# Performance work log

Measured on AMD Instinct MI355X. Metric: run time of the kernel, lower is better.

## Reference

```python
import jax, jax.numpy as jnp
import numpy as np

B, T, D, H, K = 8, 4096, 768, 12, 64
EPS_WKV = 1e-9
EPS_GN = 1e-5


def setup_inputs() -> dict:
    key = jax.random.key(0)
    ks = jax.random.split(key, 12)
    x = jax.random.normal(ks[0], (B, T, D), jnp.float32)
    # linear projection weights (torch nn.Linear stores [out, in]; y = x @ W.T)
    W_r = jax.random.normal(ks[1], (D, D), jnp.float32) * 0.02
    W_k = jax.random.normal(ks[2], (D, D), jnp.float32) * 0.02
    W_v = jax.random.normal(ks[3], (D, D), jnp.float32) * 0.02
    W_o = jax.random.normal(ks[4], (D, D), jnp.float32) * 0.02
    time_mix_r = jax.random.uniform(ks[5], (D,), jnp.float32)
    time_mix_k = jax.random.uniform(ks[6], (D,), jnp.float32)
    time_mix_v = jax.random.uniform(ks[7], (D,), jnp.float32)
    # around the module's init values (time_decay ~ -0.075, time_first ~ 0.15 at layer 6/12)
    time_decay = -0.075 + 0.1 * jax.random.normal(ks[8], (H, K), jnp.float32)
    time_first = 0.15 + 0.1 * jax.random.normal(ks[9], (H, K), jnp.float32)
    gn_weight = jnp.ones((D,), jnp.float32)
    gn_bias = jnp.zeros((D,), jnp.float32)
    return {
        "x": x,
        "time_mix_r": time_mix_r, "time_mix_k": time_mix_k, "time_mix_v": time_mix_v,
        "time_decay": time_decay, "time_first": time_first,
        "W_r": W_r, "W_k": W_k, "W_v": W_v, "W_o": W_o,
        "gn_weight": gn_weight, "gn_bias": gn_bias,
    }


def reference(x, time_mix_r, time_mix_k, time_mix_v, time_decay, time_first,
              W_r, W_k, W_v, W_o, gn_weight, gn_bias):
    Bx, Tx, Dx = x.shape
    Hx, Kx = time_decay.shape
    # token-shift: previous timestep (zero-initialized state)
    x_prev = jnp.concatenate([jnp.zeros_like(x[:, :1]), x[:, :-1]], axis=1)
    xr = x * time_mix_r + x_prev * (1.0 - time_mix_r)
    xk = x * time_mix_k + x_prev * (1.0 - time_mix_k)
    xv = x * time_mix_v + x_prev * (1.0 - time_mix_v)
    r = jax.nn.sigmoid(xr @ W_r.T).reshape(Bx, Tx, Hx, Kx)
    k = (xk @ W_k.T).reshape(Bx, Tx, Hx, Kx)
    v = (xv @ W_v.T).reshape(Bx, Tx, Hx, Kx)

    w = jnp.exp(-jnp.exp(time_decay))   # [H,K] decay per channel
    eu = jnp.exp(time_first)            # [H,K] bonus for current token

    def step(carry, kv_t):
        num, den = carry                # each [B,H,K]
        k_t, v_t = kv_t                 # each [B,H,K]
        ek = jnp.exp(k_t)
        wkv = (num + eu * ek * v_t) / (den + eu * ek + EPS_WKV)
        return (num * w + ek * v_t, den * w + ek), wkv

    k_tm = jnp.moveaxis(k, 1, 0)        # [T,B,H,K]
    v_tm = jnp.moveaxis(v, 1, 0)
    init = (jnp.zeros((Bx, Hx, Kx), x.dtype), jnp.zeros((Bx, Hx, Kx), x.dtype))
    _, wkv = jax.lax.scan(step, init, (k_tm, v_tm))
    out = jnp.moveaxis(wkv, 0, 1)       # [B,T,H,K]

    y = r * out                         # [B,T,H,K]
    # torch GroupNorm(H, D) on [B, D, T]: normalize each group over (K channels x T steps)
    mean = y.mean(axis=(1, 3), keepdims=True)
    var = y.var(axis=(1, 3), keepdims=True)
    y = (y - mean) * jax.lax.rsqrt(var + EPS_GN)
    y = y * gn_weight.reshape(1, 1, Hx, Kx) + gn_bias.reshape(1, 1, Hx, Kx)
    return y.reshape(Bx, Tx, Dx) @ W_o.T
```

## Files before the change

### kernel.cpp

```cpp
#include <hip/hip_runtime.h>
#include <hip/hip_bf16.h>
#include <cstdint>

#define B_ 8
#define T_ 4096
#define D_ 768
#define H_ 12
#define M_ (B_*T_)
#define CHUNKS 64
#define CLEN 64
#define WELEM (D_*D_)
#define NCH (B_*H_*64)

typedef __attribute__((ext_vector_type(8))) short bf16x8;
typedef __attribute__((ext_vector_type(4))) float f32x4;

static __device__ __forceinline__ unsigned short f2bf(float f) {
  __hip_bfloat16 h = __float2bfloat16(f);
  return __builtin_bit_cast(unsigned short, h);
}
static __device__ __forceinline__ float bf2f(unsigned short u) {
  unsigned v = ((unsigned)u) << 16;
  return __builtin_bit_cast(float, v);
}

static __device__ __forceinline__ void async16(const void* g, void* l) {
  __builtin_amdgcn_global_load_lds(
      (const __attribute__((address_space(1))) unsigned int*)g,
      (__attribute__((address_space(3))) unsigned int*)l, 16, 0, 0);
}

__global__ __launch_bounds__(256) void zero_out_kernel(float* __restrict__ out, size_t n4) {
  size_t gid = (size_t)blockIdx.x * 256 + threadIdx.x;
  if (gid < n4) *(float4*)(out + gid * 4) = make_float4(0.f, 0.f, 0.f, 0.f);
}

__global__ __launch_bounds__(256) void mix_kernel(
    const float* __restrict__ x, const float* __restrict__ tmr,
    const float* __restrict__ tmk, const float* __restrict__ tmv,
    unsigned short* __restrict__ xr, unsigned short* __restrict__ xk,
    unsigned short* __restrict__ xv) {
  size_t gid = (size_t)blockIdx.x * 256 + threadIdx.x;
  size_t idx4 = gid * 4;
  int d = (int)(idx4 % D_);
  size_t row = idx4 / D_;
  int t = (int)(row & (T_ - 1));
  float4 xc = *(const float4*)(x + idx4);
  float4 xp = make_float4(0.f, 0.f, 0.f, 0.f);
  if (t > 0) xp = *(const float4*)(x + idx4 - D_);
  float4 mr = *(const float4*)(tmr + d);
  float4 mk = *(const float4*)(tmk + d);
  float4 mv = *(const float4*)(tmv + d);
  ushort4 orr, okk, ovv;
  orr.x = f2bf(xc.x*mr.x + xp.x*(1.f-mr.x));
  orr.y = f2bf(xc.y*mr.y + xp.y*(1.f-mr.y));
  orr.z = f2bf(xc.z*mr.z + xp.z*(1.f-mr.z));
  orr.w = f2bf(xc.w*mr.w + xp.w*(1.f-mr.w));
  okk.x = f2bf(xc.x*mk.x + xp.x*(1.f-mk.x));
  okk.y = f2bf(xc.y*mk.y + xp.y*(1.f-mk.y));
  okk.z = f2bf(xc.z*mk.z + xp.z*(1.f-mk.z));
  okk.w = f2bf(xc.w*mk.w + xp.w*(1.f-mk.w));
  ovv.x = f2bf(xc.x*mv.x + xp.x*(1.f-mv.x));
  ovv.y = f2bf(xc.y*mv.y + xp.y*(1.f-mv.y));
  ovv.z = f2bf(xc.z*mv.z + xp.z*(1.f-mv.z));
  ovv.w = f2bf(xc.w*mv.w + xp.w*(1.f-mv.w));
  *(ushort4*)(xr + idx4) = orr;
  *(ushort4*)(xk + idx4) = okk;
  *(ushort4*)(xv + idx4) = ovv;
}

__global__ __launch_bounds__(256) void wconv_kernel(
    const float* __restrict__ a, const float* __restrict__ b,
    const float* __restrict__ c, const float* __restrict__ d,
    unsigned short* __restrict__ o) {
  size_t gid = (size_t)blockIdx.x * 256 + threadIdx.x;
  size_t idx4 = gid * 4;
  size_t mi = idx4 / WELEM;
  size_t off = idx4 % WELEM;
  const float* src = (mi == 0) ? a : (mi == 1) ? b : (mi == 2) ? c : d;
  float4 v = *(const float4*)(src + off);
  ushort4 u;
  u.x = f2bf(v.x); u.y = f2bf(v.y); u.z = f2bf(v.z); u.w = f2bf(v.w);
  *(ushort4*)(o + idx4) = u;
}

template<int ACT, int OBF>
__global__ __launch_bounds__(256) void gemm_nt(
    const unsigned short* __restrict__ A,
    const unsigned short* __restrict__ Bw,
    void* __restrict__ Cv, int M, int N, int Kd) {
  __shared__ __align__(16) unsigned short As[128 * 32];
  __shared__ __align__(16) unsigned short Bs[128 * 32];
  const int tid = threadIdx.x;
  const int wave = tid >> 6, lane = tid & 63;
  const int quad = lane >> 4, l16 = lane & 15;
  const int m0 = blockIdx.y * 128, n0 = blockIdx.x * 128;
  const int wm = (wave & 1) * 64, wn = (wave >> 1) * 64;

  f32x4 acc[4][4] = {};

  for (int kb = 0; kb < Kd; kb += 32) {
    __syncthreads();
#pragma unroll
    for (int j = 0; j < 2; ++j) {
      int chunk = wave * 128 + j * 64 + lane;
      int row = chunk >> 2, kc = chunk & 3;
      const unsigned short* ga = A  + ((size_t)(m0 + row) * Kd + kb + kc * 8);
      async16(ga, &As[chunk * 8]);
      const unsigned short* gb = Bw + ((size_t)(n0 + row) * Kd + kb + kc * 8);
      async16(gb, &Bs[chunk * 8]);
    }
    __syncthreads();

    bf16x8 a[4], b[4];
#pragma unroll
    for (int i = 0; i < 4; ++i)
      a[i] = *(const bf16x8*)&As[(wm + i * 16 + l16) * 32 + quad * 8];
#pragma unroll
    for (int i = 0; i < 4; ++i)
      b[i] = *(const bf16x8*)&Bs[(wn + i * 16 + l16) * 32 + quad * 8];
#pragma unroll
    for (int i = 0; i < 4; ++i)
#pragma unroll
      for (int j = 0; j < 4; ++j)
        acc[i][j] = __builtin_amdgcn_mfma_f32_16x16x32_bf16(a[i], b[j], acc[i][j], 0, 0, 0);
  }

#pragma unroll
  for (int i = 0; i < 4; ++i) {
    int rowb = m0 + wm + i * 16 + quad * 4;
#pragma unroll
    for (int j = 0; j < 4; ++j) {
      int col = n0 + wn + j * 16 + l16;
#pragma unroll
      for (int r = 0; r < 4; ++r) {
        float v = acc[i][j][r];
        if (ACT == 1) v = 1.f / (1.f + __expf(-v));
        size_t idx = (size_t)(rowb + r) * N + col;
        if (OBF) ((unsigned short*)Cv)[idx] = f2bf(v);
        else     ((float*)Cv)[idx] = v;
      }
    }
  }
}

__global__ __launch_bounds__(256) void wkv_pass1(
    const unsigned short* __restrict__ Kb, const unsigned short* __restrict__ Vb,
    const float* __restrict__ td,
    float* __restrict__ sumN, float* __restrict__ sumD) {
  int gid = blockIdx.x * 256 + threadIdx.x;
  int k = gid & 63;
  int h = (gid >> 6) % H_;
  int tmp = (gid >> 6) / H_;
  int b = tmp % B_;
  int c = tmp / B_;
  float w = __expf(-__expf(td[h * 64 + k]));
  size_t base = ((size_t)(b * T_ + c * CLEN)) * D_ + h * 64 + k;
  float num = 0.f, den = 0.f;
#pragma unroll 8
  for (int i = 0; i < CLEN; ++i) {
    float kk = bf2f(Kb[base + (size_t)i * D_]);
    float vv = bf2f(Vb[base + (size_t)i * D_]);
    float ek = __expf(kk);
    num = num * w + ek * vv;
    den = den * w + ek;
  }
  sumN[gid] = num;
  sumD[gid] = den;
}

__global__ __launch_bounds__(256) void wkv_pass2(
    const float* __restrict__ sumN, const float* __restrict__ sumD,
    const float* __restrict__ td,
    float* __restrict__ prefN, float* __restrict__ prefD,
    float* __restrict__ gstats) {
  int tid = blockIdx.x * 256 + threadIdx.x;
  if (blockIdx.x == 0 && threadIdx.x < 192) gstats[threadIdx.x] = 0.f;
  int k = tid & 63;
  int h = (tid >> 6) % H_;
  float w = __expf(-__expf(td[h * 64 + k]));
  float wL = w;
#pragma unroll
  for (int i = 0; i < 6; ++i) wL *= wL;
  float n = 0.f, d = 0.f;
  for (int c = 0; c < CHUNKS; ++c) {
    int j = c * NCH + tid;
    prefN[j] = n; prefD[j] = d;
    n = n * wL + sumN[j];
    d = d * wL + sumD[j];
  }
}

__global__ __launch_bounds__(256) void wkv_pass3(
    const unsigned short* __restrict__ Kb, const unsigned short* __restrict__ Vb,
    unsigned short* __restrict__ RY,
    const float* __restrict__ td, const float* __restrict__ tf,
    const float* __restrict__ prefN, const float* __restrict__ prefD,
    float* __restrict__ gsum, float* __restrict__ gsq) {
  int gid = blockIdx.x * 256 + threadIdx.x;
  int k = gid & 63;
  int h = (gid >> 6) % H_;
  int tmp = (gid >> 6) / H_;
  int b = tmp % B_;
  int c = tmp / B_;
  float w = __expf(-__expf(td[h * 64 + k]));
  float eu = __expf(tf[h * 64 + k]);
  float num = prefN[gid], den = prefD[gid];
  size_t base = ((size_t)(b * T_ + c * CLEN)) * D_ + h * 64 + k;
  float s1 = 0.f, s2 = 0.f;
#pragma unroll 4
  for (int i = 0; i < CLEN; ++i) {
    size_t idx = base + (size_t)i * D_;
    float kk = bf2f(Kb[idx]);
    float vv = bf2f(Vb[idx]);
    float rr = bf2f(RY[idx]);
    float ek = __expf(kk);
    float wkv = (num + eu * ek * vv) / (den + eu * ek + 1e-9f);
    unsigned short ybf = f2bf(rr * wkv);
    RY[idx] = ybf;
    float y = bf2f(ybf);
    s1 += y; s2 += y * y;
    num = num * w + ek * vv;
    den = den * w + ek;
  }
#pragma unroll
  for (int off = 32; off; off >>= 1) {
    s1 += __shfl_down(s1, off);
    s2 += __shfl_down(s2, off);
  }
  if (k == 0) {
    atomicAdd(&gsum[b * H_ + h], s1);
    atomicAdd(&gsq [b * H_ + h], s2);
  }
}

__global__ __launch_bounds__(256) void gn_kernel(
    const unsigned short* __restrict__ Y, const float* __restrict__ gsum,
    const float* __restrict__ gsq, const float* __restrict__ gw,
    const float* __restrict__ gb, unsigned short* __restrict__ Ybf) {
  size_t gid = (size_t)blockIdx.x * 256 + threadIdx.x;
  size_t idx4 = gid * 4;
  int d = (int)(idx4 % D_);
  size_t row = idx4 / D_;
  int b = (int)(row >> 12);
  int h = d >> 6;
  int g = b * H_ + h;
  const float inv = 1.f / (float)(T_ * 64);
  float mean = gsum[g] * inv;
  float var = gsq[g] * inv - mean * mean;
  float rstd = rsqrtf(var + 1e-5f);
  ushort4 yu = *(const ushort4*)(Y + idx4);
  float4 wv = *(const float4*)(gw + d);
  float4 bv = *(const float4*)(gb + d);
  ushort4 o;
  o.x = f2bf((bf2f(yu.x) - mean) * rstd * wv.x + bv.x);
  o.y = f2bf((bf2f(yu.y) - mean) * rstd * wv.y + bv.y);
  o.z = f2bf((bf2f(yu.z) - mean) * rstd * wv.z + bv.z);
  o.w = f2bf((bf2f(yu.w) - mean) * rstd * wv.w + bv.w);
  *(ushort4*)(Ybf + idx4) = o;
}

extern "C" void kernel_launch(void* const* d_in, const int* in_sizes, int n_in,
                              void* d_out, int out_size, void* d_ws, size_t ws_size,
                              hipStream_t stream) {
  (void)in_sizes; (void)n_in;
  const float* x   = (const float*)d_in[0];
  const float* tmr = (const float*)d_in[1];
  const float* tmk = (const float*)d_in[2];
  const float* tmv = (const float*)d_in[3];
  const float* td  = (const float*)d_in[4];
  const float* tf  = (const float*)d_in[5];
  const float* Wr  = (const float*)d_in[6];
  const float* Wk  = (const float*)d_in[7];
  const float* Wv  = (const float*)d_in[8];
  const float* Wo  = (const float*)d_in[9];
  const float* gw  = (const float*)d_in[10];
  const float* gb  = (const float*)d_in[11];
  float* out = (float*)d_out;

  constexpr size_t MD = (size_t)M_ * D_;
  constexpr size_t NEED = 4 * (MD * 2)
                        + (size_t)4 * WELEM * 2
                        + 4 * ((size_t)CHUNKS * NCH * 4)
                        + 1024;
  if (ws_size < NEED) {
    zero_out_kernel<<<(int)((MD / 4 + 255) / 256), 256, 0, stream>>>(out, MD / 4);
    return;
  }

  char* ws = (char*)d_ws;
  unsigned short* XR = (unsigned short*)ws; ws += MD * 2;
  unsigned short* XK = (unsigned short*)ws; ws += MD * 2;
  unsigned short* XV = (unsigned short*)ws; ws += MD * 2;
  unsigned short* Rb = (unsigned short*)ws; ws += MD * 2;
  unsigned short* Wb = (unsigned short*)ws; ws += (size_t)4 * WELEM * 2;
  float* sumN  = (float*)ws; ws += (size_t)CHUNKS * NCH * 4;
  float* sumD  = (float*)ws; ws += (size_t)CHUNKS * NCH * 4;
  float* prefN = (float*)ws; ws += (size_t)CHUNKS * NCH * 4;
  float* prefD = (float*)ws; ws += (size_t)CHUNKS * NCH * 4;
  float* gstats = (float*)ws; ws += 1024;
  unsigned short* Kb = XR;
  unsigned short* Vb = XK;
  unsigned short* Yb = XV;

  mix_kernel<<<(int)(MD / 1024), 256, 0, stream>>>(x, tmr, tmk, tmv, XR, XK, XV);
  wconv_kernel<<<(4 * WELEM / 4) / 256, 256, 0, stream>>>(Wr, Wk, Wv, Wo, Wb);

  dim3 ggrid(D_ / 128, M_ / 128);
  gemm_nt<1, 1><<<ggrid, 256, 0, stream>>>(XR, Wb,             Rb, M_, D_, D_);
  gemm_nt<0, 1><<<ggrid, 256, 0, stream>>>(XK, Wb + WELEM,     Kb, M_, D_, D_);
  gemm_nt<0, 1><<<ggrid, 256, 0, stream>>>(XV, Wb + 2 * WELEM, Vb, M_, D_, D_);

  wkv_pass1<<<(CHUNKS * NCH) / 256, 256, 0, stream>>>(Kb, Vb, td, sumN, sumD);
  wkv_pass2<<<NCH / 256, 256, 0, stream>>>(sumN, sumD, td, prefN, prefD, gstats);
  wkv_pass3<<<(CHUNKS * NCH) / 256, 256, 0, stream>>>(Kb, Vb, Rb, td, tf,
                                                      prefN, prefD, gstats, gstats + 96);
  gn_kernel<<<(int)(MD / 1024), 256, 0, stream>>>(Rb, gstats, gstats + 96, gw, gb, Yb);

  gemm_nt<0, 0><<<ggrid, 256, 0, stream>>>(Yb, Wb + 3 * WELEM, out, M_, D_, D_);
}
```

Before: 579.0 us.

## Double-buffer GEMM, interleave R/K/V into one buffer, split mix kernel

The GEMM now double-buffers its LDS tiles with async global-to-LDS loads and explicit waitcnt/barriers, so the next K-slice loads while MFMAs run. It also remaps blocks so each XCD handles contiguous M strips, and stages bf16 outputs through LDS for 16-byte coalesced stores. R, K and V are written interleaved into one [M, 3D] buffer, which the WKV passes read together. The mix kernel is split into three single-output launches that reuse one workspace buffer, and the prefix pass updates its arrays in place. Together these cut workspace size and aim to overlap memory latency with compute, at the cost of more kernel launches and re-reading x three times.

```diff
diff --git a/kernel.cpp b/kernel.cpp
--- a/kernel.cpp
+++ b/kernel.cpp
@@ -9,8 +9,9 @@
 #define M_ (B_*T_)
 #define CHUNKS 64
 #define CLEN 64
+#define NCH (B_*H_*64)
+#define NF 2304
 #define WELEM (D_*D_)
-#define NCH (B_*H_*64)
 
 typedef __attribute__((ext_vector_type(8))) short bf16x8;
 typedef __attribute__((ext_vector_type(4))) float f32x4;
@@ -35,11 +36,9 @@
   if (gid < n4) *(float4*)(out + gid * 4) = make_float4(0.f, 0.f, 0.f, 0.f);
 }
 
-__global__ __launch_bounds__(256) void mix_kernel(
-    const float* __restrict__ x, const float* __restrict__ tmr,
-    const float* __restrict__ tmk, const float* __restrict__ tmv,
-    unsigned short* __restrict__ xr, unsigned short* __restrict__ xk,
-    unsigned short* __restrict__ xv) {
+__global__ __launch_bounds__(256) void mix_one_kernel(
+    const float* __restrict__ x, const float* __restrict__ tm,
+    unsigned short* __restrict__ o) {
   size_t gid = (size_t)blockIdx.x * 256 + threadIdx.x;
   size_t idx4 = gid * 4;
   int d = (int)(idx4 % D_);
@@ -48,25 +47,13 @@
   float4 xc = *(const float4*)(x + idx4);
   float4 xp = make_float4(0.f, 0.f, 0.f, 0.f);
   if (t > 0) xp = *(const float4*)(x + idx4 - D_);
-  float4 mr = *(const float4*)(tmr + d);
-  float4 mk = *(const float4*)(tmk + d);
-  float4 mv = *(const float4*)(tmv + d);
-  ushort4 orr, okk, ovv;
-  orr.x = f2bf(xc.x*mr.x + xp.x*(1.f-mr.x));
-  orr.y = f2bf(xc.y*mr.y + xp.y*(1.f-mr.y));
-  orr.z = f2bf(xc.z*mr.z + xp.z*(1.f-mr.z));
-  orr.w = f2bf(xc.w*mr.w + xp.w*(1.f-mr.w));
-  okk.x = f2bf(xc.x*mk.x + xp.x*(1.f-mk.x));
-  okk.y = f2bf(xc.y*mk.y + xp.y*(1.f-mk.y));
-  okk.z = f2bf(xc.z*mk.z + xp.z*(1.f-mk.z));
-  okk.w = f2bf(xc.w*mk.w + xp.w*(1.f-mk.w));
-  ovv.x = f2bf(xc.x*mv.x + xp.x*(1.f-mv.x));
-  ovv.y = f2bf(xc.y*mv.y + xp.y*(1.f-mv.y));
-  ovv.z = f2bf(xc.z*mv.z + xp.z*(1.f-mv.z));
-  ovv.w = f2bf(xc.w*mv.w + xp.w*(1.f-mv.w));
-  *(ushort4*)(xr + idx4) = orr;
-  *(ushort4*)(xk + idx4) = okk;
-  *(ushort4*)(xv + idx4) = ovv;
+  float4 m = *(const float4*)(tm + d);
+  ushort4 u;
+  u.x = f2bf(xp.x + m.x * (xc.x - xp.x));
+  u.y = f2bf(xp.y + m.y * (xc.y - xp.y));
+  u.z = f2bf(xp.z + m.z * (xc.z - xp.z));
+  u.w = f2bf(xp.w + m.w * (xc.w - xp.w));
+  *(ushort4*)(o + idx4) = u;
 }
 
 __global__ __launch_bounds__(256) void wconv_kernel(
@@ -84,69 +71,126 @@
   *(ushort4*)(o + idx4) = u;
 }
 
-template<int ACT, int OBF>
-__global__ __launch_bounds__(256) void gemm_nt(
+#define EPI_LD 136
+template<int SIG, int OBF>
+__global__ __launch_bounds__(256) void gemm_bt(
     const unsigned short* __restrict__ A,
     const unsigned short* __restrict__ Bw,
-    void* __restrict__ Cv, int M, int N, int Kd) {
-  __shared__ __align__(16) unsigned short As[128 * 32];
-  __shared__ __align__(16) unsigned short Bs[128 * 32];
+    void* __restrict__ Cv, int ldc, int col0) {
+  constexpr int SMEM = OBF ? (128 * EPI_LD) : 16384;
+  __shared__ __align__(16) unsigned short smem[SMEM < 16384 ? 16384 : SMEM];
+
+  const int flat = blockIdx.x;
+  const int xcd = flat & 7;
+  const int s = flat >> 3;
+  const int strip = xcd * 32 + s / 6;
+  const int nt = s % 6;
+  const int m0 = strip * 128, n0 = nt * 128;
+
   const int tid = threadIdx.x;
   const int wave = tid >> 6, lane = tid & 63;
   const int quad = lane >> 4, l16 = lane & 15;
-  const int m0 = blockIdx.y * 128, n0 = blockIdx.x * 128;
   const int wm = (wave & 1) * 64, wn = (wave >> 1) * 64;
 
+  const int ch0 = wave * 128 + lane;
+  const int ch1 = ch0 + 64;
+  const int r0 = ch0 >> 2, k0c = (ch0 & 3) * 8;
+  const int r1 = ch1 >> 2, k1c = (ch1 & 3) * 8;
+  const unsigned short* ga0 = A  + ((size_t)(m0 + r0)) * D_ + k0c;
+  const unsigned short* ga1 = A  + ((size_t)(m0 + r1)) * D_ + k1c;
+  const unsigned short* gb0 = Bw + ((size_t)(n0 + r0)) * D_ + k0c;
+  const unsigned short* gb1 = Bw + ((size_t)(n0 + r1)) * D_ + k1c;
+
   f32x4 acc[4][4] = {};
 
-  for (int kb = 0; kb < Kd; kb += 32) {
+  {
+    unsigned short* As = smem;
+    unsigned short* Bs = smem + 4096;
+    async16(ga0, &As[ch0 * 8]);
+    async16(ga1, &As[ch1 * 8]);
+    async16(gb0, &Bs[ch0 * 8]);
+    async16(gb1, &Bs[ch1 * 8]);
+  }
+  asm volatile("s_waitcnt vmcnt(0)" ::: "memory");
+  asm volatile("s_barrier" ::: "memory");
+
+  const int NI = D_ / 32;
+  for (int i = 0; i < NI; ++i) {
+    const int cb = i & 1;
+    if (i + 1 < NI) {
+      const int kb = (i + 1) * 32;
+      unsigned short* As = smem + (cb ^ 1) * 8192;
+      unsigned short* Bs = As + 4096;
+      async16(ga0 + kb, &As[ch0 * 8]);
+      async16(ga1 + kb, &As[ch1 * 8]);
+      async16(gb0 + kb, &Bs[ch0 * 8]);
+      async16(gb1 + kb, &Bs[ch1 * 8]);
+      asm volatile("s_waitcnt vmcnt(4)" ::: "memory");
+    } else {
+      asm volatile("s_waitcnt vmcnt(0)" ::: "memory");
+    }
+    asm volatile("s_barrier" ::: "memory");
+
+    const unsigned short* As = smem + cb * 8192;
+    const unsigned short* Bs = As + 4096;
+    bf16x8 a[4], b[4];
+#pragma unroll
+    for (int ii = 0; ii < 4; ++ii)
+      a[ii] = *(const bf16x8*)&As[(wm + ii * 16 + l16) * 32 + quad * 8];
+#pragma unroll
+    for (int ii = 0; ii < 4; ++ii)
+      b[ii] = *(const bf16x8*)&Bs[(wn + ii * 16 + l16) * 32 + quad * 8];
+#pragma unroll
+    for (int ii = 0; ii < 4; ++ii)
+#pragma unroll
+      for (int jj = 0; jj < 4; ++jj)
+        acc[ii][jj] = __builtin_amdgcn_mfma_f32_16x16x32_bf16(a[ii], b[jj], acc[ii][jj], 0, 0, 0);
+
+    asm volatile("s_barrier" ::: "memory");
+  }
+
+  if (OBF) {
     __syncthreads();
 #pragma unroll
-    for (int j = 0; j < 2; ++j) {
-      int chunk = wave * 128 + j * 64 + lane;
-      int row = chunk >> 2, kc = chunk & 3;
-      const unsigned short* ga = A  + ((size_t)(m0 + row) * Kd + kb + kc * 8);
-      async16(ga, &As[chunk * 8]);
-      const unsigned short* gb = Bw + ((size_t)(n0 + row) * Kd + kb + kc * 8);
-      async16(gb, &Bs[chunk * 8]);
+    for (int ii = 0; ii < 4; ++ii)
+#pragma unroll
+      for (int jj = 0; jj < 4; ++jj)
+#pragma unroll
+        for (int r = 0; r < 4; ++r) {
+          float v = acc[ii][jj][r];
+          if (SIG) v = 1.f / (1.f + __expf(-v));
+          smem[(wm + ii * 16 + quad * 4 + r) * EPI_LD + wn + jj * 16 + l16] = f2bf(v);
+        }
+    __syncthreads();
+    unsigned short* C = (unsigned short*)Cv;
+#pragma unroll
+    for (int sdx = 0; sdx < 8; ++sdx) {
+      int cid = sdx * 256 + tid;
+      int row = cid >> 4, c8 = cid & 15;
+      bf16x8 val = *(const bf16x8*)&smem[row * EPI_LD + c8 * 8];
+      *(bf16x8*)(C + (size_t)(m0 + row) * ldc + col0 + n0 + c8 * 8) = val;
     }
-    __syncthreads();
-
-    bf16x8 a[4], b[4];
-#pragma unroll
-    for (int i = 0; i < 4; ++i)
-      a[i] = *(const bf16x8*)&As[(wm + i * 16 + l16) * 32 + quad * 8];
-#pragma unroll
-    for (int i = 0; i < 4; ++i)
-      b[i] = *(const bf16x8*)&Bs[(wn + i * 16 + l16) * 32 + quad * 8];
-#pragma unroll
-    for (int i = 0; i < 4; ++i)
-#pragma unroll
-      for (int j = 0; j < 4; ++j)
-        acc[i][j] = __builtin_amdgcn_mfma_f32_16x16x32_bf16(a[i], b[j], acc[i][j], 0, 0, 0);
-  }
-
-#pragma unroll
-  for (int i = 0; i < 4; ++i) {
-    int rowb = m0 + wm + i * 16 + quad * 4;
-#pragma unroll
-    for (int j = 0; j < 4; ++j) {
-      int col = n0 + wn + j * 16 + l16;
-#pragma unroll
-      for (int r = 0; r < 4; ++r) {
-        float v = acc[i][j][r];
-        if (ACT == 1) v = 1.f / (1.f + __expf(-v));
-        size_t idx = (size_t)(rowb + r) * N + col;
-        if (OBF) ((unsigned short*)Cv)[idx] = f2bf(v);
-        else     ((float*)Cv)[idx] = v;
+  } else {
+    float* C = (float*)Cv;
+#pragma unroll
+    for (int ii = 0; ii < 4; ++ii) {
+      int rowb = m0 + wm + ii * 16 + quad * 4;
+#pragma unroll
+      for (int jj = 0; jj < 4; ++jj) {
+        int col = col0 + n0 + wn + jj * 16 + l16;
+#pragma unroll
+        for (int r = 0; r < 4; ++r) {
+          float v = acc[ii][jj][r];
+          if (SIG) v = 1.f / (1.f + __expf(-v));
+          C[(size_t)(rowb + r) * ldc + col] = v;
+        }
       }
     }
   }
 }
 
 __global__ __launch_bounds__(256) void wkv_pass1(
-    const unsigned short* __restrict__ Kb, const unsigned short* __restrict__ Vb,
-    const float* __restrict__ td,
+    const unsigned short* __restrict__ RKV, const float* __restrict__ td,
     float* __restrict__ sumN, float* __restrict__ sumD) {
   int gid = blockIdx.x * 256 + threadIdx.x;
   int k = gid & 63;
@@ -155,12 +199,13 @@
   int b = tmp % B_;
   int c = tmp / B_;
   float w = __expf(-__expf(td[h * 64 + k]));
-  size_t base = ((size_t)(b * T_ + c * CLEN)) * D_ + h * 64 + k;
+  const unsigned short* Kp =
+      RKV + ((size_t)(b * T_ + c * CLEN)) * NF + D_ + h * 64 + k;
   float num = 0.f, den = 0.f;
 #pragma unroll 8
   for (int i = 0; i < CLEN; ++i) {
-    float kk = bf2f(Kb[base + (size_t)i * D_]);
-    float vv = bf2f(Vb[base + (size_t)i * D_]);
+    float kk = bf2f(Kp[(size_t)i * NF]);
+    float vv = bf2f(Kp[(size_t)i * NF + D_]);
     float ek = __expf(kk);
     num = num * w + ek * vv;
     den = den * w + ek;
@@ -170,10 +215,8 @@
 }
 
 __global__ __launch_bounds__(256) void wkv_pass2(
-    const float* __restrict__ sumN, const float* __restrict__ sumD,
-    const float* __restrict__ td,
-    float* __restrict__ prefN, float* __restrict__ prefD,
-    float* __restrict__ gstats) {
+    float* __restrict__ sumN, float* __restrict__ sumD,
+    const float* __restrict__ td, float* __restrict__ gstats) {
   int tid = blockIdx.x * 256 + threadIdx.x;
   if (blockIdx.x == 0 && threadIdx.x < 192) gstats[threadIdx.x] = 0.f;
   int k = tid & 63;
@@ -185,15 +228,15 @@
   float n = 0.f, d = 0.f;
   for (int c = 0; c < CHUNKS; ++c) {
     int j = c * NCH + tid;
-    prefN[j] = n; prefD[j] = d;
-    n = n * wL + sumN[j];
-    d = d * wL + sumD[j];
+    float sn = sumN[j], sd = sumD[j];
+    sumN[j] = n; sumD[j] = d;
+    n = n * wL + sn;
+    d = d * wL + sd;
   }
 }
 
 __global__ __launch_bounds__(256) void wkv_pass3(
-    const unsigned short* __restrict__ Kb, const unsigned short* __restrict__ Vb,
-    unsigned short* __restrict__ RY,
+    unsigned short* __restrict__ RKV,
     const float* __restrict__ td, const float* __restrict__ tf,
     const float* __restrict__ prefN, const float* __restrict__ prefD,
     float* __restrict__ gsum, float* __restrict__ gsq) {
@@ -206,18 +249,18 @@
   float w = __expf(-__expf(td[h * 64 + k]));
   float eu = __expf(tf[h * 64 + k]);
   float num = prefN[gid], den = prefD[gid];
-  size_t base = ((size_t)(b * T_ + c * CLEN)) * D_ + h * 64 + k;
+  unsigned short* Rp = RKV + ((size_t)(b * T_ + c * CLEN)) * NF + h * 64 + k;
   float s1 = 0.f, s2 = 0.f;
 #pragma unroll 4
   for (int i = 0; i < CLEN; ++i) {
-    size_t idx = base + (size_t)i * D_;
-    float kk = bf2f(Kb[idx]);
-    float vv = bf2f(Vb[idx]);
-    float rr = bf2f(RY[idx]);
+    size_t off = (size_t)i * NF;
+    float rr = bf2f(Rp[off]);
+    float kk = bf2f(Rp[off + D_]);
+    float vv = bf2f(Rp[off + 2 * D_]);
     float ek = __expf(kk);
     float wkv = (num + eu * ek * vv) / (den + eu * ek + 1e-9f);
     unsigned short ybf = f2bf(rr * wkv);
-    RY[idx] = ybf;
+    Rp[off] = ybf;
     float y = bf2f(ybf);
     s1 += y; s2 += y * y;
     num = num * w + ek * vv;
@@ -235,9 +278,9 @@
 }
 
 __global__ __launch_bounds__(256) void gn_kernel(
-    const unsigned short* __restrict__ Y, const float* __restrict__ gsum,
+    const unsigned short* __restrict__ RKV, const float* __restrict__ gsum,
     const float* __restrict__ gsq, const float* __restrict__ gw,
-    const float* __restrict__ gb, unsigned short* __restrict__ Ybf) {
+    const float* __restrict__ gb, unsigned short* __restrict__ Yb) {
   size_t gid = (size_t)blockIdx.x * 256 + threadIdx.x;
   size_t idx4 = gid * 4;
   int d = (int)(idx4 % D_);
@@ -249,7 +292,7 @@
   float mean = gsum[g] * inv;
   float var = gsq[g] * inv - mean * mean;
   float rstd = rsqrtf(var + 1e-5f);
-  ushort4 yu = *(const ushort4*)(Y + idx4);
+  ushort4 yu = *(const ushort4*)(RKV + row * NF + d);
   float4 wv = *(const float4*)(gw + d);
   float4 bv = *(const float4*)(gb + d);
   ushort4 o;
@@ -257,13 +300,13 @@
   o.y = f2bf((bf2f(yu.y) - mean) * rstd * wv.y + bv.y);
   o.z = f2bf((bf2f(yu.z) - mean) * rstd * wv.z + bv.z);
   o.w = f2bf((bf2f(yu.w) - mean) * rstd * wv.w + bv.w);
-  *(ushort4*)(Ybf + idx4) = o;
+  *(ushort4*)(Yb + idx4) = o;
 }
 
 extern "C" void kernel_launch(void* const* d_in, const int* in_sizes, int n_in,
                               void* d_out, int out_size, void* d_ws, size_t ws_size,
                               hipStream_t stream) {
-  (void)in_sizes; (void)n_in;
+  (void)in_sizes; (void)n_in; (void)out_size;
   const float* x   = (const float*)d_in[0];
   const float* tmr = (const float*)d_in[1];
   const float* tmk = (const float*)d_in[2];
@@ -278,44 +321,42 @@
   const float* gb  = (const float*)d_in[11];
   float* out = (float*)d_out;
 
-  constexpr size_t MD = (size_t)M_ * D_;
-  constexpr size_t NEED = 4 * (MD * 2)
-                        + (size_t)4 * WELEM * 2
-                        + 4 * ((size_t)CHUNKS * NCH * 4)
-                        + 1024;
+  constexpr size_t MD    = (size_t)M_ * D_;
+  constexpr size_t RKV_E = (size_t)M_ * NF;
+  constexpr size_t NEED  = MD * 2
+                         + RKV_E * 2
+                         + (size_t)4 * WELEM * 2
+                         + 2 * ((size_t)CHUNKS * NCH * 4)
+                         + 1024;
   if (ws_size < NEED) {
     zero_out_kernel<<<(int)((MD / 4 + 255) / 256), 256, 0, stream>>>(out, MD / 4);
     return;
   }
 
   char* ws = (char*)d_ws;
-  unsigned short* XR = (unsigned short*)ws; ws += MD * 2;
-  unsigned short* XK = (unsigned short*)ws; ws += MD * 2;
-  unsigned short* XV = (unsigned short*)ws; ws += MD * 2;
-  unsigned short* Rb = (unsigned short*)ws; ws += MD * 2;
-  unsigned short* Wb = (unsigned short*)ws; ws += (size_t)4 * WELEM * 2;
-  float* sumN  = (float*)ws; ws += (size_t)CHUNKS * NCH * 4;
-  float* sumD  = (float*)ws; ws += (size_t)CHUNKS * NCH * 4;
-  float* prefN = (float*)ws; ws += (size_t)CHUNKS * NCH * 4;
-  float* prefD = (float*)ws; ws += (size_t)CHUNKS * NCH * 4;
+  unsigned short* mixb = (unsigned short*)ws; ws += MD * 2;
+  unsigned short* RKV  = (unsigned short*)ws; ws += RKV_E * 2;
+  unsigned short* Wb   = (unsigned short*)ws; ws += (size_t)4 * WELEM * 2;
+  float* sumN   = (float*)ws; ws += (size_t)CHUNKS * NCH * 4;
+  float* sumD   = (float*)ws; ws += (size_t)CHUNKS * NCH * 4;
   float* gstats = (float*)ws; ws += 1024;
-  unsigned short* Kb = XR;
-  unsigned short* Vb = XK;
-  unsigned short* Yb = XV;
-
-  mix_kernel<<<(int)(MD / 1024), 256, 0, stream>>>(x, tmr, tmk, tmv, XR, XK, XV);
+  unsigned short* Yb = mixb;
+
   wconv_kernel<<<(4 * WELEM / 4) / 256, 256, 0, stream>>>(Wr, Wk, Wv, Wo, Wb);
 
-  dim3 ggrid(D_ / 128, M_ / 128);
-  gemm_nt<1, 1><<<ggrid, 256, 0, stream>>>(XR, Wb,             Rb, M_, D_, D_);
-  gemm_nt<0, 1><<<ggrid, 256, 0, stream>>>(XK, Wb + WELEM,     Kb, M_, D_, D_);
-  gemm_nt<0, 1><<<ggrid, 256, 0, stream>>>(XV, Wb + 2 * WELEM, Vb, M_, D_, D_);
-
-  wkv_pass1<<<(CHUNKS * NCH) / 256, 256, 0, stream>>>(Kb, Vb, td, sumN, sumD);
-  wkv_pass2<<<NCH / 256, 256, 0, stream>>>(sumN, sumD, td, prefN, prefD, gstats);
-  wkv_pass3<<<(CHUNKS * NCH) / 256, 256, 0, stream>>>(Kb, Vb, Rb, td, tf,
-                                                      prefN, prefD, gstats, gstats + 96);
-  gn_kernel<<<(int)(MD / 1024), 256, 0, stream>>>(Rb, gstats, gstats + 96, gw, gb, Yb);
-
-  gemm_nt<0, 0><<<ggrid, 256, 0, stream>>>(Yb, Wb + 3 * WELEM, out, M_, D_, D_);
-}
+  const int mgrid = (int)(MD / 1024);
+  mix_one_kernel<<<mgrid, 256, 0, stream>>>(x, tmr, mixb);
+  gemm_bt<1, 1><<<1536, 256, 0, stream>>>(mixb, Wb,             (void*)RKV, NF, 0);
+  mix_one_kernel<<<mgrid, 256, 0, stream>>>(x, tmk, mixb);
+  gemm_bt<0, 1><<<1536, 256, 0, stream>>>(mixb, Wb + WELEM,     (void*)RKV, NF, D_);
+  mix_one_kernel<<<mgrid, 256, 0, stream>>>(x, tmv, mixb);
+  gemm_bt<0, 1><<<1536, 256, 0, stream>>>(mixb, Wb + 2 * WELEM, (void*)RKV, NF, 2 * D_);
+
+  wkv_pass1<<<(CHUNKS * NCH) / 256, 256, 0, stream>>>(RKV, td, sumN, sumD);
+  wkv_pass2<<<NCH / 256, 256, 0, stream>>>(sumN, sumD, td, gstats);
+  wkv_pass3<<<(CHUNKS * NCH) / 256, 256, 0, stream>>>(RKV, td, tf, sumN, sumD,
+                                                      gstats, gstats + 96);
+  gn_kernel<<<mgrid, 256, 0, stream>>>(RKV, gstats, gstats + 96, gw, gb, Yb);
+
+  gemm_bt<0, 0><<<1536, 256, 0, stream>>>(Yb, Wb + 3 * WELEM, (void*)out, D_, 0);
+}
```

Result: no change. 585.8 us (+1.2%).
